# Optimization experiments

Hardware: AMD Instinct MI355X
Metric: run time of the kernel (lower is better)

## Reference

```python
import jax, jax.numpy as jnp
import numpy as np

D = 256; NH = 8; NL = 4; NP = 4; DH = D // NH; DFFN = 1024; NQ = 900; BS = 4
SPATIAL = ((92, 92), (46, 46), (23, 23), (12, 12))  # (H, W) per level
LEVEL_START = (0, 8464, 10580, 11109)
S = sum(h * w for h, w in SPATIAL)  # 11253


def _ln(x, g, b):
    m = jnp.mean(x, -1, keepdims=True)
    v = jnp.var(x, -1, keepdims=True)
    return (x - m) / jnp.sqrt(v + 1e-5) * g + b


def setup_inputs() -> dict:
    key = jax.random.key(0)
    ks = jax.random.split(key, 24)
    p = lambda k, s: 0.02 * jax.random.normal(k, s, jnp.float32)
    return {
        "tgt": jax.random.normal(ks[0], (NQ, BS, D), jnp.float32),
        "tgt_query_pos": jax.random.normal(ks[1], (NQ, BS, D), jnp.float32),
        "tgt_reference_points": jax.random.uniform(ks[2], (NQ, BS, NL, 2), jnp.float32),
        "memory": jax.random.normal(ks[3], (S, BS, D), jnp.float32),
        "memory_spatial_shapes": jnp.array(SPATIAL, jnp.int32),
        "memory_level_start_index": jnp.array(LEVEL_START, jnp.int32),
        "in_proj_w": p(ks[4], (3 * D, D)), "in_proj_b": p(ks[5], (3 * D,)),
        "out_proj_w": p(ks[6], (D, D)), "out_proj_b": p(ks[7], (D,)),
        "off_w": p(ks[8], (NH * NL * NP * 2, D)), "off_b": p(ks[9], (NH * NL * NP * 2,)),
        "aw_w": p(ks[10], (NH * NL * NP, D)), "aw_b": p(ks[11], (NH * NL * NP,)),
        "vproj_w": p(ks[12], (D, D)), "vproj_b": p(ks[13], (D,)),
        "oproj_w": p(ks[14], (D, D)), "oproj_b": p(ks[15], (D,)),
        "ln1_g": jnp.ones((D,), jnp.float32), "ln1_b": jnp.zeros((D,), jnp.float32),
        "ln2_g": jnp.ones((D,), jnp.float32), "ln2_b": jnp.zeros((D,), jnp.float32),
        "ln3_g": jnp.ones((D,), jnp.float32), "ln3_b": jnp.zeros((D,), jnp.float32),
        "lin1_w": p(ks[16], (DFFN, D)), "lin1_b": p(ks[17], (DFFN,)),
        "lin2_w": p(ks[18], (D, DFFN)), "lin2_b": p(ks[19], (D,)),
    }


def _self_attn(q, k, v, in_w, in_b, out_w, out_b):
    # q, k, v: (nq, bs, d) -- torch nn.MultiheadAttention, eval mode
    wq, wk, wv = jnp.split(in_w, 3, axis=0)
    bq, bk, bv = jnp.split(in_b, 3)
    qp = (q @ wq.T + bq).reshape(NQ, BS, NH, DH)
    kp = (k @ wk.T + bk).reshape(NQ, BS, NH, DH)
    vp = (v @ wv.T + bv).reshape(NQ, BS, NH, DH)
    s = jnp.einsum("qbhd,kbhd->bhqk", qp, kp) / jnp.sqrt(jnp.float32(DH))
    a = jax.nn.softmax(s, axis=-1)
    o = jnp.einsum("bhqk,kbhd->qbhd", a, vp).reshape(NQ, BS, D)
    return o @ out_w.T + out_b


def _msdeform(x, ref, mem, off_w, off_b, aw_w, aw_b, vproj_w, vproj_b, oproj_w, oproj_b):
    # x: (bs, nq, d); ref: (bs, nq, nl, 2) in [0,1]; mem: (bs, S, d)
    value = (mem @ vproj_w.T + vproj_b).reshape(BS, S, NH, DH)
    off = (x @ off_w.T + off_b).reshape(BS, NQ, NH, NL, NP, 2)
    aw = jax.nn.softmax((x @ aw_w.T + aw_b).reshape(BS, NQ, NH, NL * NP), axis=-1)
    aw = aw.reshape(BS, NQ, NH, NL, NP)
    # offset normalizer = (W, H) per level
    norm = jnp.array([[w, h] for (h, w) in SPATIAL], jnp.float32)
    loc = ref[:, :, None, :, None, :] + off / norm[None, None, None, :, None, :]
    out = jnp.zeros((BS, NH, NQ, DH), x.dtype)
    for l, (H, W) in enumerate(SPATIAL):
        s0 = LEVEL_START[l]
        v = value[:, s0:s0 + H * W].transpose(0, 2, 1, 3)  # (bs, nh, H*W, dh)
        g = loc[:, :, :, l].transpose(0, 2, 1, 3, 4)       # (bs, nh, nq, np, 2)
        # grid_sample align_corners=False, padding_mode='zeros'
        px = g[..., 0] * W - 0.5
        py = g[..., 1] * H - 0.5
        x0 = jnp.floor(px).astype(jnp.int32)
        y0 = jnp.floor(py).astype(jnp.int32)
        wx = px - x0
        wy = py - y0
        samp = jnp.zeros((BS, NH, NQ, NP, DH), x.dtype)
        for dx, dy, w in ((0, 0, (1 - wx) * (1 - wy)), (1, 0, wx * (1 - wy)),
                          (0, 1, (1 - wx) * wy), (1, 1, wx * wy)):
            xi = x0 + dx
            yi = y0 + dy
            valid = ((xi >= 0) & (xi < W) & (yi >= 0) & (yi < H)).astype(x.dtype)
            idx = (jnp.clip(yi, 0, H - 1) * W + jnp.clip(xi, 0, W - 1)).reshape(BS, NH, NQ * NP)
            gat = jnp.take_along_axis(v, idx[..., None], axis=2).reshape(BS, NH, NQ, NP, DH)
            samp = samp + (w * valid)[..., None] * gat
        a = aw[:, :, :, l].transpose(0, 2, 1, 3)  # (bs, nh, nq, np)
        out = out + (samp * a[..., None]).sum(axis=3)
    out = out.transpose(0, 2, 1, 3).reshape(BS, NQ, D)
    return out @ oproj_w.T + oproj_b


def reference(tgt, tgt_query_pos, tgt_reference_points, memory,
              memory_spatial_shapes, memory_level_start_index,
              in_proj_w, in_proj_b, out_proj_w, out_proj_b,
              off_w, off_b, aw_w, aw_b, vproj_w, vproj_b, oproj_w, oproj_b,
              ln1_g, ln1_b, ln2_g, ln2_b, ln3_g, ln3_b,
              lin1_w, lin1_b, lin2_w, lin2_b):
    # module_seq = ['sa', 'ca', 'ffn']; dropout inactive (eval)
    q = tgt + tgt_query_pos
    tgt2 = _self_attn(q, q, tgt, in_proj_w, in_proj_b, out_proj_w, out_proj_b)
    tgt = _ln(tgt + tgt2, ln2_g, ln2_b)
    x = (tgt + tgt_query_pos).transpose(1, 0, 2)
    ref = tgt_reference_points.transpose(1, 0, 2, 3)
    mem = memory.transpose(1, 0, 2)
    tgt2 = _msdeform(x, ref, mem, off_w, off_b, aw_w, aw_b,
                     vproj_w, vproj_b, oproj_w, oproj_b).transpose(1, 0, 2)
    tgt = _ln(tgt + tgt2, ln1_g, ln1_b)
    ff = jax.nn.relu(tgt @ lin1_w.T + lin1_b) @ lin2_w.T + lin2_b
    return _ln(tgt + ff, ln3_g, ln3_b)
```

## Files before the change

### kernel.cpp

```cpp
#include <hip/hip_runtime.h>
#include <math.h>

#define D_MODEL 256
#define NHEAD   8
#define NLVL    4
#define NPTS    4
#define DHEAD   32
#define DFFN    1024
#define NQ      900
#define BSZ     4
#define NROW    (NQ * BSZ)
#define NROWP   3648
#define S_TOT   11253
#define VROWS   (S_TOT * BSZ)
#define SASCALE 0.17677669529663687f

typedef __attribute__((ext_vector_type(8))) short short8;
typedef __attribute__((ext_vector_type(4))) float f32x4;
typedef unsigned short ushort_t;

static __device__ __forceinline__ unsigned f2bf1(float f) {
    unsigned u = __float_as_uint(f);
    return (u + 0x7FFFu + ((u >> 16) & 1u)) >> 16;
}
static __device__ __forceinline__ unsigned pack2bf(float x, float y) {
    return f2bf1(x) | (f2bf1(y) << 16);
}
static __device__ __forceinline__ float bf2f(ushort_t u) {
    return __uint_as_float(((unsigned)u) << 16);
}

#if __has_builtin(__builtin_amdgcn_global_load_lds)
#define HAS_GLL 1
#endif

static __device__ __forceinline__ void stage_w16(const ushort_t* g, ushort_t* ldsbase, int lane)
{
#ifdef HAS_GLL
    __builtin_amdgcn_global_load_lds(
        (const __attribute__((address_space(1))) unsigned int*)g,
        (__attribute__((address_space(3))) unsigned int*)ldsbase, 16, 0, 0);
#else
    *(uint4*)(ldsbase + lane * 8) = *(const uint4*)g;
#endif
}

#define WB_IN   0
#define WB_VP   196608
#define WB_OUTP 262144
#define WB_OFF  327680
#define WB_AW   393216
#define WB_OP   425984
#define WB_L1   491520
#define WB_L2   753664
#define WB_TOT  1015808

__global__ __launch_bounds__(256) void cvt_weights(
    const float* __restrict__ w_in, const float* __restrict__ w_vp,
    const float* __restrict__ w_outp, const float* __restrict__ w_off,
    const float* __restrict__ w_aw, const float* __restrict__ w_op,
    const float* __restrict__ w_l1, const float* __restrict__ w_l2,
    ushort_t* __restrict__ dst,
    const float* __restrict__ tgt, const float* __restrict__ qpos,
    ushort_t* __restrict__ tgt16, ushort_t* __restrict__ tq16)
{
    int b = blockIdx.x;
    if (b < 496) {
        const float* src;
        int dstoff;
        int kbits = 8;
        if (b < 96)       { src = w_in;   dstoff = WB_IN;   }
        else if (b < 128) { src = w_vp;   b -= 96;  dstoff = WB_VP;   }
        else if (b < 160) { src = w_outp; b -= 128; dstoff = WB_OUTP; }
        else if (b < 192) { src = w_off;  b -= 160; dstoff = WB_OFF;  }
        else if (b < 208) { src = w_aw;   b -= 192; dstoff = WB_AW;   }
        else if (b < 240) { src = w_op;   b -= 208; dstoff = WB_OP;   }
        else if (b < 368) { src = w_l1;   b -= 240; dstoff = WB_L1;   }
        else              { src = w_l2;   b -= 368; dstoff = WB_L2;   kbits = 10; }
        int i = (b * 256 + threadIdx.x) * 8;
        float4 f0 = *(const float4*)(src + i);
        float4 f1 = *(const float4*)(src + i + 4);
        uint4 u;
        u.x = pack2bf(f0.x, f0.y); u.y = pack2bf(f0.z, f0.w);
        u.z = pack2bf(f1.x, f1.y); u.w = pack2bf(f1.z, f1.w);
        int K = 1 << kbits;
        int n = i >> kbits;
        int k = i & (K - 1);
        int kswz = (k & ~63) | ((k & 63) ^ ((n & 7) << 3));
        *(uint4*)(dst + dstoff + (size_t)n * K + kswz) = u;
    } else {
        int bb = b - 496;
        ushort_t* dbuf = tgt16;
        bool addq = false;
        if (bb >= 456) { bb -= 456; dbuf = tq16; addq = true; }
        int i = bb * 2048 + threadIdx.x * 8;
        int row = i >> 8, k = i & 255;
        uint4 u = make_uint4(0u, 0u, 0u, 0u);
        if (row < NROW) {
            const float* sp = tgt + (size_t)row * 256 + k;
            float4 f0 = *(const float4*)(sp + 0);
            float4 f1 = *(const float4*)(sp + 4);
            if (addq) {
                const float* qp = qpos + (size_t)row * 256 + k;
                float4 q0 = *(const float4*)(qp + 0);
                float4 q1 = *(const float4*)(qp + 4);
                f0.x += q0.x; f0.y += q0.y; f0.z += q0.z; f0.w += q0.w;
                f1.x += q1.x; f1.y += q1.y; f1.z += q1.z; f1.w += q1.w;
            }
            u.x = pack2bf(f0.x, f0.y); u.y = pack2bf(f0.z, f0.w);
            u.z = pack2bf(f1.x, f1.y); u.w = pack2bf(f1.z, f1.w);
        }
        int kswz = (k & ~63) | ((k & 63) ^ ((row & 7) << 3));
        *(uint4*)(dbuf + (size_t)row * 256 + kswz) = u;
    }
}

__global__ __launch_bounds__(256) void proj_fused(
    const ushort_t* __restrict__ tq16, const ushort_t* __restrict__ tgt16,
    const ushort_t* __restrict__ in_wb, const float* __restrict__ in_b,
    const float* __restrict__ mem, const ushort_t* __restrict__ vp_wb,
    const float* __restrict__ vp_b,
    ushort_t* __restrict__ qkv16, ushort_t* __restrict__ value16)
{
    __shared__ ushort_t As[2][64 * 64];
    __shared__ ushort_t Ws[2][256 * 64];

    const int t    = threadIdx.x;
    const int bid  = blockIdx.x;
    const int wv   = t >> 6;
    const int ln   = t & 63;
    const int L    = ln & 15;
    const int quad = ln >> 4;
    const int swz  = (L & 7) << 3;
    const int lrow = ln >> 3;
    const int lchk = (ln & 7) << 3;

    if (bid < 684) {
        const int m0 = (bid % 57) * 64;
        const int n0 = (bid / 57) * 64;
        const float oscale = (n0 < 256) ? SASCALE : 1.f;
        const ushort_t* Ab = (n0 < 512) ? tq16 : tgt16;

        auto stageQ = [&](int k0, int buf) {
#pragma unroll
            for (int j = 0; j < 2; ++j) {
                int r0 = (wv * 2 + j) * 8;
                stage_w16(Ab + (size_t)(m0 + r0 + lrow) * 256 + k0 + lchk, &As[buf][r0 * 64], ln);
                stage_w16(in_wb + (size_t)(n0 + r0 + lrow) * 256 + k0 + lchk, &Ws[buf][r0 * 64], ln);
            }
        };

        f32x4 acc[4] = {{0.f,0.f,0.f,0.f},{0.f,0.f,0.f,0.f},
                        {0.f,0.f,0.f,0.f},{0.f,0.f,0.f,0.f}};

        stageQ(0, 0);
        __syncthreads();
        int cur = 0;
        for (int k = 0; k < 4; ++k) {
            if (k < 3) stageQ((k + 1) * 64, cur ^ 1);
#pragma unroll
            for (int kh = 0; kh < 2; ++kh) {
                int ko = (kh * 32 + quad * 8) ^ swz;
                short8 af = *(const short8*)&As[cur][(wv * 16 + L) * 64 + ko];
#pragma unroll
                for (int cb = 0; cb < 4; ++cb) {
                    short8 bf = *(const short8*)&Ws[cur][(cb * 16 + L) * 64 + ko];
                    acc[cb] = __builtin_amdgcn_mfma_f32_16x16x32_bf16(af, bf, acc[cb], 0, 0, 0);
                }
            }
            __syncthreads();
            cur ^= 1;
        }
#pragma unroll
        for (int cb = 0; cb < 4; ++cb) {
            int col = n0 + cb * 16 + L;
            float bv = in_b[col];
#pragma unroll
            for (int i = 0; i < 4; ++i) {
                int m = m0 + wv * 16 + quad * 4 + i;
                if (m < NROW)
                    qkv16[(size_t)m * 768 + col] = (ushort_t)f2bf1((acc[cb][i] + bv) * oscale);
            }
        }
    } else {
        const int vb = bid - 684;
        const int m0 = vb * 64;
        const int trow = t >> 2;
        const int tk   = (t & 3) << 4;
        const int wsz  = (trow & 7) << 3;

        const int  mrow = m0 + trow;
        const bool mv   = (mrow < VROWS);
        const float* arow = mem + (size_t)mrow * 256 + tk;

        auto stageWv = [&](int k0, int buf) {
#pragma unroll
            for (int j = 0; j < 8; ++j) {
                int r0 = (wv * 8 + j) * 8;
                stage_w16(vp_wb + (size_t)(r0 + lrow) * 256 + k0 + lchk, &Ws[buf][r0 * 64], ln);
            }
        };
        auto stageAv = [&](int k0, int buf) {
            uint4 u0, u1;
            if (mv) {
                const float* ap = arow + k0;
                float4 a0 = *(const float4*)(ap + 0);
                float4 a1 = *(const float4*)(ap + 4);
                float4 a2 = *(const float4*)(ap + 8);
                float4 a3 = *(const float4*)(ap + 12);
                u0.x = pack2bf(a0.x, a0.y); u0.y = pack2bf(a0.z, a0.w);
                u0.z = pack2bf(a1.x, a1.y); u0.w = pack2bf(a1.z, a1.w);
                u1.x = pack2bf(a2.x, a2.y); u1.y = pack2bf(a2.z, a2.w);
                u1.z = pack2bf(a3.x, a3.y); u1.w = pack2bf(a3.z, a3.w);
            } else {
                u0 = make_uint4(0u, 0u, 0u, 0u); u1 = u0;
            }
            *(uint4*)&As[buf][trow * 64 + (tk ^ wsz)]       = u0;
            *(uint4*)&As[buf][trow * 64 + ((tk + 8) ^ wsz)] = u1;
        };

        f32x4 acc[16];
#pragma unroll
        for (int i = 0; i < 16; ++i) acc[i] = (f32x4){0.f, 0.f, 0.f, 0.f};

        stageWv(0, 0);
        stageAv(0, 0);
        __syncthreads();
        int cur = 0;
        for (int k = 0; k < 4; ++k) {
            if (k < 3) stageWv((k + 1) * 64, cur ^ 1);
#pragma unroll
            for (int kh = 0; kh < 2; ++kh) {
                int ko = (kh * 32 + quad * 8) ^ swz;
                short8 af = *(const short8*)&As[cur][(wv * 16 + L) * 64 + ko];
#pragma unroll
                for (int cb = 0; cb < 16; ++cb) {
                    short8 bf = *(const short8*)&Ws[cur][(cb * 16 + L) * 64 + ko];
                    acc[cb] = __builtin_amdgcn_mfma_f32_16x16x32_bf16(af, bf, acc[cb], 0, 0, 0);
                }
            }
            if (k < 3) stageAv((k + 1) * 64, cur ^ 1);
            __syncthreads();
            cur ^= 1;
        }

        ushort_t* Cs = Ws[0];
#pragma unroll
        for (int half = 0; half < 2; ++half) {
            if (half) __syncthreads();
#pragma unroll
            for (int cb = 0; cb < 8; ++cb) {
                int col = cb * 16 + L;
                float bv = vp_b[half * 128 + col];
#pragma unroll
                for (int i = 0; i < 4; ++i) {
                    int r = wv * 16 + quad * 4 + i;
                    Cs[r * 136 + col] = (ushort_t)f2bf1(acc[half * 8 + cb][i] + bv);
                }
            }
            __syncthreads();
            {
                int r  = t >> 2;
                int ch = (t & 3) * 32;
                int m  = m0 + r;
                if (m < VROWS) {
                    const ushort_t* src = &Cs[r * 136 + ch];
                    uint4* dst = (uint4*)(value16 + (size_t)m * 256 + half * 128 + ch);
#pragma unroll
                    for (int j = 0; j < 4; ++j)
                        dst[j] = *(const uint4*)(src + j * 8);
                }
            }
        }
    }
}

__global__ __launch_bounds__(256) void sa_flash16(
    const ushort_t* __restrict__ qkv, ushort_t* __restrict__ attn_out)
{
    __shared__ ushort_t Ks[2 * 2080];
    __shared__ ushort_t Vt[2 * 2304];
    __shared__ ushort_t Ps[4 * 1152];

    const int t    = threadIdx.x;
    const int q0   = blockIdx.x * 64;
    const int b    = blockIdx.y & 3;
    const int h    = blockIdx.y >> 2;
    const int wv   = t >> 6;
    const int ln   = t & 63;
    const int L    = ln & 15;
    const int quad = ln >> 4;

    union { uint4 u; short8 s; } qu;
    qu.u = make_uint4(0u, 0u, 0u, 0u);
    {
        int q = q0 + wv * 16 + L;
        if (q < NQ)
            qu.u = *(const uint4*)(qkv + ((size_t)q * 4 + b) * 768 + h * 32 + quad * 8);
    }
    const short8 qf = qu.s;

    float mrun = -1e30f, lrun = 0.f;
    f32x4 oacc[2] = {{0.f,0.f,0.f,0.f},{0.f,0.f,0.f,0.f}};

    const int skey = t >> 2;
    const int sdg  = t & 3;

    uint4 ku, vu;
    auto kv_load = [&](int k0) {
        int kg = k0 + skey;
        ku = make_uint4(0u, 0u, 0u, 0u);
        vu = make_uint4(0u, 0u, 0u, 0u);
        if (kg < NQ) {
            const ushort_t* base = qkv + ((size_t)kg * 4 + b) * 768 + 256 + h * 32 + sdg * 8;
            ku = *(const uint4*)base;
            vu = *(const uint4*)(base + 256);
        }
    };

    kv_load(0);
    int it = 0;
    for (int k0 = 0; k0 < NQ; k0 += 64, it ^= 1) {
        *(uint4*)&Ks[it * 2080 + sdg * 520 + skey * 8] = ku;
        {
            ushort_t* vp = &Vt[it * 2304 + sdg * 8 * 72 + skey];
            vp[0 * 72] = (ushort_t)(vu.x & 0xffffu);
            vp[1 * 72] = (ushort_t)(vu.x >> 16);
            vp[2 * 72] = (ushort_t)(vu.y & 0xffffu);
            vp[3 * 72] = (ushort_t)(vu.y >> 16);
            vp[4 * 72] = (ushort_t)(vu.z & 0xffffu);
            vp[5 * 72] = (ushort_t)(vu.z >> 16);
            vp[6 * 72] = (ushort_t)(vu.w & 0xffffu);
            vp[7 * 72] = (ushort_t)(vu.w >> 16);
        }
        __syncthreads();
        if (k0 + 64 < NQ) kv_load(k0 + 64);

        f32x4 sacc[4] = {{0.f,0.f,0.f,0.f},{0.f,0.f,0.f,0.f},
                         {0.f,0.f,0.f,0.f},{0.f,0.f,0.f,0.f}};
#pragma unroll
        for (int cb = 0; cb < 4; ++cb) {
            short8 kf = *(const short8*)&Ks[it * 2080 + quad * 520 + (cb * 16 + L) * 8];
            sacc[cb] = __builtin_amdgcn_mfma_f32_16x16x32_bf16(kf, qf, sacc[cb], 0, 0, 0);
        }
        if (k0 + 64 > NQ) {
#pragma unroll
            for (int cb = 0; cb < 4; ++cb)
#pragma unroll
                for (int i = 0; i < 4; ++i)
                    if (k0 + cb * 16 + quad * 4 + i >= NQ) sacc[cb][i] = -1e30f;
        }

        float ml = -1e30f;
#pragma unroll
        for (int cb = 0; cb < 4; ++cb)
#pragma unroll
            for (int i = 0; i < 4; ++i) ml = fmaxf(ml, sacc[cb][i]);
        ml = fmaxf(ml, __shfl_xor(ml, 16, 64));
        ml = fmaxf(ml, __shfl_xor(ml, 32, 64));
        float mnew  = fmaxf(mrun, ml);
        float alpha = __expf(mrun - mnew);
        float p[16];
        float rs = 0.f;
#pragma unroll
        for (int cb = 0; cb < 4; ++cb)
#pragma unroll
            for (int i = 0; i < 4; ++i) {
                float e = __expf(sacc[cb][i] - mnew);
                p[cb * 4 + i] = e;
                rs += e;
            }
        rs += __shfl_xor(rs, 16, 64);
        rs += __shfl_xor(rs, 32, 64);
        lrun = lrun * alpha + rs;
        mrun = mnew;

        {
            ushort_t* pw = &Ps[wv * 1152 + L * 72];
#pragma unroll
            for (int cb = 0; cb < 4; ++cb) {
                uint2 u;
                u.x = pack2bf(p[cb * 4 + 0], p[cb * 4 + 1]);
                u.y = pack2bf(p[cb * 4 + 2], p[cb * 4 + 3]);
                *(uint2*)&pw[cb * 16 + quad * 4] = u;
            }
        }
#pragma unroll
        for (int i = 0; i < 4; ++i) {
            float ai = __shfl(alpha, quad * 4 + i, 64);
            oacc[0][i] *= ai;
            oacc[1][i] *= ai;
        }
        __syncthreads();

#pragma unroll
        for (int ks = 0; ks < 2; ++ks) {
            short8 pf = *(const short8*)&Ps[wv * 1152 + L * 72 + ks * 32 + quad * 8];
#pragma unroll
            for (int db = 0; db < 2; ++db) {
                short8 vf = *(const short8*)&Vt[it * 2304 + (db * 16 + L) * 72 + ks * 32 + quad * 8];
                oacc[db] = __builtin_amdgcn_mfma_f32_16x16x32_bf16(pf, vf, oacc[db], 0, 0, 0);
            }
        }
    }

#pragma unroll
    for (int i = 0; i < 4; ++i) {
        float lq = __shfl(lrun, quad * 4 + i, 64);
        float li = 1.f / lq;
        int q = q0 + wv * 16 + quad * 4 + i;
        if (q < NQ) {
            ushort_t* op = attn_out + ((size_t)q * 4 + b) * 256 + h * 32 + L;
            op[0]  = (ushort_t)f2bf1(oacc[0][i] * li);
            op[16] = (ushort_t)f2bf1(oacc[1][i] * li);
        }
    }
}

__global__ __launch_bounds__(512, 1) void fused_ca(
    const ushort_t* __restrict__ att16,
    const float* __restrict__ tgt, const float* __restrict__ qpos,
    const ushort_t* __restrict__ outp_wb, const float* __restrict__ outp_b,
    const float* __restrict__ ln2g, const float* __restrict__ ln2b,
    const ushort_t* __restrict__ off_wb, const float* __restrict__ off_b,
    const ushort_t* __restrict__ aw_wb, const float* __restrict__ aw_b,
    const float* __restrict__ refp,
    float* __restrict__ tgt_a, float* __restrict__ px_g,
    float* __restrict__ py_g, float* __restrict__ aw_g)
{
    __shared__ ushort_t Ws[2][256 * 64];
    __shared__ ushort_t att_s[16 * 264];
    __shared__ ushort_t xca_s[16 * 264];
    __shared__ float    aws_s[16 * 128];
    __shared__ float    sS[8][16], s2S[8][16];

    const int t    = threadIdx.x;
    const int m0   = blockIdx.x * 16;
    const int wv   = t >> 6;
    const int ln   = t & 63;
    const int L    = ln & 15;
    const int quad = ln >> 4;
    const int swz  = (L & 7) << 3;
    const int lrow = ln >> 3;
    const int lchk = (ln & 7) << 3;
    const int rloc = quad * 4;

    auto stage4 = [&](const ushort_t* base, int buf) {
#pragma unroll
        for (int j = 0; j < 4; ++j) {
            int r0 = (wv * 4 + j) * 8;
            stage_w16(base + (size_t)(r0 + lrow) * 256 + lchk, &Ws[buf][r0 * 64], ln);
        }
    };
    auto stage2 = [&](const ushort_t* base, int buf) {
#pragma unroll
        for (int j = 0; j < 2; ++j) {
            int r0 = (wv * 2 + j) * 8;
            stage_w16(base + (size_t)(r0 + lrow) * 256 + lchk, &Ws[buf][r0 * 64], ln);
        }
    };
    auto mfma2 = [&](const ushort_t* A, int koff, int buf, f32x4* acc) {
#pragma unroll
        for (int kh = 0; kh < 2; ++kh) {
            int ko = (kh * 32 + quad * 8) ^ swz;
            short8 af = *(const short8*)&A[L * 264 + koff + kh * 32 + quad * 8];
#pragma unroll
            for (int cb = 0; cb < 2; ++cb) {
                short8 bf = *(const short8*)&Ws[buf][(wv * 32 + cb * 16 + L) * 64 + ko];
                acc[cb] = __builtin_amdgcn_mfma_f32_16x16x32_bf16(af, bf, acc[cb], 0, 0, 0);
            }
        }
    };

    {
        int r = t >> 5, s = (t & 31) * 8;
        *(uint4*)&att_s[r * 264 + s] = *(const uint4*)(att16 + (size_t)(m0 + r) * 256 + s);
    }
    stage4(outp_wb, 0);
    __syncthreads();
    int cur = 0;

    {
        f32x4 acc[2] = {{0.f,0.f,0.f,0.f},{0.f,0.f,0.f,0.f}};
        for (int k = 0; k < 4; ++k) {
            if (k < 3) stage4(outp_wb + (k + 1) * 64, cur ^ 1);
            else       stage4(off_wb, cur ^ 1);
            mfma2(att_s, k * 64, cur, acc);
            __syncthreads();
            cur ^= 1;
        }
        float s[4] = {0.f,0.f,0.f,0.f}, s2v[4] = {0.f,0.f,0.f,0.f};
#pragma unroll
        for (int cb = 0; cb < 2; ++cb) {
            int col = wv * 32 + cb * 16 + L;
            float bv = outp_b[col];
#pragma unroll
            for (int i = 0; i < 4; ++i) {
                float xv = acc[cb][i] + bv + tgt[(size_t)(m0 + rloc + i) * 256 + col];
                acc[cb][i] = xv;
                s[i] += xv; s2v[i] += xv * xv;
            }
        }
#pragma unroll
        for (int off = 1; off < 16; off <<= 1)
#pragma unroll
            for (int i = 0; i < 4; ++i) {
                s[i]   += __shfl_xor(s[i],   off, 64);
                s2v[i] += __shfl_xor(s2v[i], off, 64);
            }
        if (L == 0)
#pragma unroll
            for (int i = 0; i < 4; ++i) { sS[wv][rloc + i] = s[i]; s2S[wv][rloc + i] = s2v[i]; }
        __syncthreads();
        float mean[4], rstd[4];
#pragma unroll
        for (int i = 0; i < 4; ++i) {
            float St = 0.f, S2t = 0.f;
#pragma unroll
            for (int w = 0; w < 8; ++w) { St += sS[w][rloc + i]; S2t += s2S[w][rloc + i]; }
            mean[i] = St * (1.f / 256.f);
            float var = S2t * (1.f / 256.f) - mean[i] * mean[i];
            rstd[i] = rsqrtf(var + 1e-5f);
        }
#pragma unroll
        for (int cb = 0; cb < 2; ++cb) {
            int col = wv * 32 + cb * 16 + L;
            float gv = ln2g[col], bt = ln2b[col];
#pragma unroll
            for (int i = 0; i < 4; ++i) {
                float y = (acc[cb][i] - mean[i]) * rstd[i] * gv + bt;
                tgt_a[(size_t)(m0 + rloc + i) * 256 + col] = y;
                xca_s[(rloc + i) * 264 + col] =
                    (ushort_t)f2bf1(y + qpos[(size_t)(m0 + rloc + i) * 256 + col]);
            }
        }
        __syncthreads();
    }

    {
        f32x4 acc[2] = {{0.f,0.f,0.f,0.f},{0.f,0.f,0.f,0.f}};
        for (int k = 0; k < 4; ++k) {
            if (k < 3) stage4(off_wb + (k + 1) * 64, cur ^ 1);
            else       stage2(aw_wb, cur ^ 1);
            mfma2(xca_s, k * 64, cur, acc);
            __syncthreads();
            cur ^= 1;
        }
        const float dims[4] = {92.f, 46.f, 23.f, 12.f};
#pragma unroll
        for (int cb = 0; cb < 2; ++cb) {
            int col = wv * 32 + cb * 16 + L;
            float bv = off_b[col];
            int hh = col >> 5, lp = (col & 31) >> 1, isY = col & 1;
            int l = lp >> 2;
            float dim = dims[l];
            float* dst = isY ? py_g : px_g;
#pragma unroll
            for (int i = 0; i < 4; ++i) {
                int row = m0 + rloc + i;
                float ref = refp[((size_t)row * 4 + l) * 2 + isY];
                dst[(size_t)row * 128 + hh * 16 + lp] = ref * dim + (acc[cb][i] + bv) - 0.5f;
            }
        }
    }

    {
        f32x4 acc = {0.f, 0.f, 0.f, 0.f};
        for (int k = 0; k < 4; ++k) {
            if (k < 3) stage2(aw_wb + (k + 1) * 64, cur ^ 1);
#pragma unroll
            for (int kh = 0; kh < 2; ++kh) {
                int ko = (kh * 32 + quad * 8) ^ swz;
                short8 af = *(const short8*)&xca_s[L * 264 + k * 64 + kh * 32 + quad * 8];
                short8 bf = *(const short8*)&Ws[cur][(wv * 16 + L) * 64 + ko];
                acc = __builtin_amdgcn_mfma_f32_16x16x32_bf16(af, bf, acc, 0, 0, 0);
            }
            __syncthreads();
            cur ^= 1;
        }
        {
            int col = wv * 16 + L;
            float bv = aw_b[col];
#pragma unroll
            for (int i = 0; i < 4; ++i)
                aws_s[(rloc + i) * 128 + col] = acc[i] + bv;
        }
        __syncthreads();
    }

    if (t < 128) {
        int r = t >> 3, hh = t & 7;
        float v[16];
        float m = -1e30f;
#pragma unroll
        for (int j = 0; j < 16; ++j) { v[j] = aws_s[r * 128 + hh * 16 + j]; m = fmaxf(m, v[j]); }
        float ssum = 0.f;
#pragma unroll
        for (int j = 0; j < 16; ++j) { v[j] = __expf(v[j] - m); ssum += v[j]; }
        float inv = 1.f / ssum;
#pragma unroll
        for (int j = 0; j < 16; ++j)
            aw_g[(size_t)(m0 + r) * 128 + hh * 16 + j] = v[j] * inv;
    }
}

__global__ __launch_bounds__(256) void msdeform4(
    const float* __restrict__ px_g, const float* __restrict__ py_g,
    const float* __restrict__ aw_g, const ushort_t* __restrict__ value16,
    ushort_t* __restrict__ out)
{
    const int t   = threadIdx.x;
    const int row = blockIdx.x * 4 + (t >> 6);
    const int ln  = t & 63;
    const int h   = ln >> 3;
    const int d   = (ln & 7) * 4;
    const int b   = row & 3;

    const int HsI[4] = {92, 46, 23, 12};
    const int S0_[4] = {0, 8464, 10580, 11109};

    const ushort_t* vb = value16 + (size_t)b * 256 + h * 32 + d;
    const float* pxr = px_g + (size_t)row * 128 + h * 16;
    const float* pyr = py_g + (size_t)row * 128 + h * 16;
    const float* awr = aw_g + (size_t)row * 128 + h * 16;

    float a0 = 0.f, a1 = 0.f, a2 = 0.f, a3 = 0.f;
#pragma unroll
    for (int l = 0; l < 4; ++l) {
        const int H = HsI[l], W = HsI[l], base = S0_[l];
#pragma unroll
        for (int p = 0; p < 4; ++p) {
            const int lp = l * 4 + p;
            float px = pxr[lp], py = pyr[lp], aw = awr[lp];
            float x0f = floorf(px), y0f = floorf(py);
            int x0 = (int)x0f, y0 = (int)y0f;
            float wx = px - x0f, wy = py - y0f;
            float s0 = 0.f, s1 = 0.f, s2 = 0.f, s3 = 0.f;
#pragma unroll
            for (int dy = 0; dy < 2; ++dy) {
#pragma unroll
                for (int dx = 0; dx < 2; ++dx) {
                    int xi = x0 + dx, yi = y0 + dy;
                    float flag = (xi >= 0 && xi < W && yi >= 0 && yi < H) ? 1.f : 0.f;
                    int xc = xi < 0 ? 0 : (xi >= W ? W - 1 : xi);
                    int yc = yi < 0 ? 0 : (yi >= H ? H - 1 : yi);
                    float wgt = (dx ? wx : 1.f - wx) * (dy ? wy : 1.f - wy) * flag;
                    uint2 gv = *(const uint2*)(vb + (size_t)(base + yc * W + xc) * 1024);
                    s0 = fmaf(wgt, bf2f((ushort_t)(gv.x & 0xffffu)), s0);
                    s1 = fmaf(wgt, bf2f((ushort_t)(gv.x >> 16)), s1);
                    s2 = fmaf(wgt, bf2f((ushort_t)(gv.y & 0xffffu)), s2);
                    s3 = fmaf(wgt, bf2f((ushort_t)(gv.y >> 16)), s3);
                }
            }
            a0 = fmaf(aw, s0, a0);
            a1 = fmaf(aw, s1, a1);
            a2 = fmaf(aw, s2, a2);
            a3 = fmaf(aw, s3, a3);
        }
    }
    uint2 u;
    u.x = pack2bf(a0, a1);
    u.y = pack2bf(a2, a3);
    *(uint2*)(out + (size_t)row * 256 + h * 32 + d) = u;
}

__global__ __launch_bounds__(512, 1) void ffn_fused(
    const ushort_t* __restrict__ att2_16,
    const float* __restrict__ tgt_a,
    const ushort_t* __restrict__ op_wb, const float* __restrict__ op_b,
    const float* __restrict__ ln1g, const float* __restrict__ ln1b,
    const ushort_t* __restrict__ l1_wb, const float* __restrict__ l1b,
    const ushort_t* __restrict__ l2_wb, const float* __restrict__ l2b,
    const float* __restrict__ ln3g, const float* __restrict__ ln3b,
    float* __restrict__ out)
{
    __shared__ ushort_t Ws[2][256 * 64];
    __shared__ ushort_t A1[16 * 264];
    __shared__ ushort_t hc[16 * 264];
    __shared__ float    sS[8][16], s2S[8][16];

    const int t    = threadIdx.x;
    const int m0   = blockIdx.x * 16;
    const int wv   = t >> 6;
    const int ln   = t & 63;
    const int L    = ln & 15;
    const int quad = ln >> 4;
    const int swz  = (L & 7) << 3;
    const int lrow = ln >> 3;
    const int lchk = (ln & 7) << 3;
    const int rloc = quad * 4;

    auto stageWs = [&](const ushort_t* base, int stride, int buf) {
#pragma unroll
        for (int j = 0; j < 4; ++j) {
            int r0 = (wv * 4 + j) * 8;
            stage_w16(base + (size_t)(r0 + lrow) * stride + lchk, &Ws[buf][r0 * 64], ln);
        }
    };
    auto mfma2 = [&](const ushort_t* A, int koff, int buf, f32x4* acc) {
#pragma unroll
        for (int kh = 0; kh < 2; ++kh) {
            int ko = (kh * 32 + quad * 8) ^ swz;
            short8 af = *(const short8*)&A[L * 264 + koff + kh * 32 + quad * 8];
#pragma unroll
            for (int cb = 0; cb < 2; ++cb) {
                short8 bf = *(const short8*)&Ws[buf][(wv * 32 + cb * 16 + L) * 64 + ko];
                acc[cb] = __builtin_amdgcn_mfma_f32_16x16x32_bf16(af, bf, acc[cb], 0, 0, 0);
            }
        }
    };

    {
        int r = t >> 5, s = (t & 31) * 8;
        *(uint4*)&hc[r * 264 + s] = *(const uint4*)(att2_16 + (size_t)(m0 + r) * 256 + s);
    }
    stageWs(op_wb, 256, 0);
    __syncthreads();
    int cur = 0;

    f32x4 resid[2];

    {
        f32x4 acc[2] = {{0.f,0.f,0.f,0.f},{0.f,0.f,0.f,0.f}};
        for (int k = 0; k < 4; ++k) {
            if (k < 3) stageWs(op_wb + (k + 1) * 64, 256, cur ^ 1);
            else       stageWs(l1_wb, 256, cur ^ 1);
            mfma2(hc, k * 64, cur, acc);
            __syncthreads();
            cur ^= 1;
        }
        float s[4] = {0.f,0.f,0.f,0.f}, s2v[4] = {0.f,0.f,0.f,0.f};
#pragma unroll
        for (int cb = 0; cb < 2; ++cb) {
            int col = wv * 32 + cb * 16 + L;
            float bv = op_b[col];
#pragma unroll
            for (int i = 0; i < 4; ++i) {
                float xv = acc[cb][i] + bv + tgt_a[(size_t)(m0 + rloc + i) * 256 + col];
                acc[cb][i] = xv;
                s[i] += xv; s2v[i] += xv * xv;
            }
        }
#pragma unroll
        for (int off = 1; off < 16; off <<= 1)
#pragma unroll
            for (int i = 0; i < 4; ++i) {
                s[i]   += __shfl_xor(s[i],   off, 64);
                s2v[i] += __shfl_xor(s2v[i], off, 64);
            }
        if (L == 0)
#pragma unroll
            for (int i = 0; i < 4; ++i) { sS[wv][rloc + i] = s[i]; s2S[wv][rloc + i] = s2v[i]; }
        __syncthreads();
        float mean[4], rstd[4];
#pragma unroll
        for (int i = 0; i < 4; ++i) {
            float St = 0.f, S2t = 0.f;
#pragma unroll
            for (int w = 0; w < 8; ++w) { St += sS[w][rloc + i]; S2t += s2S[w][rloc + i]; }
            mean[i] = St * (1.f / 256.f);
            float var = S2t * (1.f / 256.f) - mean[i] * mean[i];
            rstd[i] = rsqrtf(var + 1e-5f);
        }
#pragma unroll
        for (int cb = 0; cb < 2; ++cb) {
            int col = wv * 32 + cb * 16 + L;
            float gv = ln1g[col], bt = ln1b[col];
#pragma unroll
            for (int i = 0; i < 4; ++i) {
                float y = (acc[cb][i] - mean[i]) * rstd[i] * gv + bt;
                resid[cb][i] = y;
                A1[(rloc + i) * 264 + col] = (ushort_t)f2bf1(y);
            }
        }
        __syncthreads();
    }

    f32x4 accf[2] = {{0.f,0.f,0.f,0.f},{0.f,0.f,0.f,0.f}};
    for (int c = 0; c < 4; ++c) {
        f32x4 acch[2] = {{0.f,0.f,0.f,0.f},{0.f,0.f,0.f,0.f}};
        for (int k = 0; k < 4; ++k) {
            if (k < 3) stageWs(l1_wb + (size_t)(c * 256) * 256 + (k + 1) * 64, 256, cur ^ 1);
            else       stageWs(l2_wb + c * 256, 1024, cur ^ 1);
            mfma2(A1, k * 64, cur, acch);
            __syncthreads();
            cur ^= 1;
        }
#pragma unroll
        for (int cb = 0; cb < 2; ++cb) {
            int colc = wv * 32 + cb * 16 + L;
            float bv = l1b[c * 256 + colc];
#pragma unroll
            for (int i = 0; i < 4; ++i)
                hc[(rloc + i) * 264 + colc] = (ushort_t)f2bf1(fmaxf(acch[cb][i] + bv, 0.f));
        }
        __syncthreads();
        for (int k = 0; k < 4; ++k) {
            if (k < 3)      stageWs(l2_wb + c * 256 + (k + 1) * 64, 1024, cur ^ 1);
            else if (c < 3) stageWs(l1_wb + (size_t)((c + 1) * 256) * 256, 256, cur ^ 1);
            mfma2(hc, k * 64, cur, accf);
            __syncthreads();
            cur ^= 1;
        }
    }

    {
        float s[4] = {0.f,0.f,0.f,0.f}, s2v[4] = {0.f,0.f,0.f,0.f};
#pragma unroll
        for (int cb = 0; cb < 2; ++cb) {
            int col = wv * 32 + cb * 16 + L;
            float bv = l2b[col];
#pragma unroll
            for (int i = 0; i < 4; ++i) {
                float xv = accf[cb][i] + bv + resid[cb][i];
                accf[cb][i] = xv;
                s[i] += xv; s2v[i] += xv * xv;
            }
        }
#pragma unroll
        for (int off = 1; off < 16; off <<= 1)
#pragma unroll
            for (int i = 0; i < 4; ++i) {
                s[i]   += __shfl_xor(s[i],   off, 64);
                s2v[i] += __shfl_xor(s2v[i], off, 64);
            }
        if (L == 0)
#pragma unroll
            for (int i = 0; i < 4; ++i) { sS[wv][rloc + i] = s[i]; s2S[wv][rloc + i] = s2v[i]; }
        __syncthreads();
        float mean[4], rstd[4];
#pragma unroll
        for (int i = 0; i < 4; ++i) {
            float St = 0.f, S2t = 0.f;
#pragma unroll
            for (int w = 0; w < 8; ++w) { St += sS[w][rloc + i]; S2t += s2S[w][rloc + i]; }
            mean[i] = St * (1.f / 256.f);
            float var = S2t * (1.f / 256.f) - mean[i] * mean[i];
            rstd[i] = rsqrtf(var + 1e-5f);
        }
#pragma unroll
        for (int cb = 0; cb < 2; ++cb) {
            int col = wv * 32 + cb * 16 + L;
            float gv = ln3g[col], bt = ln3b[col];
#pragma unroll
            for (int i = 0; i < 4; ++i) {
                float y = (accf[cb][i] - mean[i]) * rstd[i] * gv + bt;
                out[(size_t)(m0 + rloc + i) * 256 + col] = y;
            }
        }
    }
}

extern "C" void kernel_launch(void* const* d_in, const int* in_sizes, int n_in,
                              void* d_out, int out_size, void* d_ws, size_t ws_size,
                              hipStream_t stream)
{
    const float* tgt    = (const float*)d_in[0];
    const float* qpos   = (const float*)d_in[1];
    const float* refp   = (const float*)d_in[2];
    const float* mem    = (const float*)d_in[3];
    const float* in_w   = (const float*)d_in[6];
    const float* in_b   = (const float*)d_in[7];
    const float* outp_w = (const float*)d_in[8];
    const float* outp_b = (const float*)d_in[9];
    const float* off_w  = (const float*)d_in[10];
    const float* off_b  = (const float*)d_in[11];
    const float* aw_w   = (const float*)d_in[12];
    const float* aw_b   = (const float*)d_in[13];
    const float* vp_w   = (const float*)d_in[14];
    const float* vp_b   = (const float*)d_in[15];
    const float* op_w   = (const float*)d_in[16];
    const float* op_b   = (const float*)d_in[17];
    const float* ln1g   = (const float*)d_in[18];
    const float* ln1b   = (const float*)d_in[19];
    const float* ln2g   = (const float*)d_in[20];
    const float* ln2b   = (const float*)d_in[21];
    const float* ln3g   = (const float*)d_in[22];
    const float* ln3b   = (const float*)d_in[23];
    const float* l1w    = (const float*)d_in[24];
    const float* l1b    = (const float*)d_in[25];
    const float* l2w    = (const float*)d_in[26];
    const float* l2b    = (const float*)d_in[27];
    float* out = (float*)d_out;
    float* ws  = (float*)d_ws;

    ushort_t* qkv16    = (ushort_t*)ws;
    ushort_t* att16    = (ushort_t*)(ws + 691200);
    float*    tgt_a    = ws + 1843200;
    ushort_t* tgt16    = (ushort_t*)(ws + 1843200);
    ushort_t* tq16     = (ushort_t*)(ws + 2310144);
    float*    px_g     = ws + 2995200;
    float*    py_g     = ws + 3456000;
    float*    aw_g     = ws + 3916800;
    ushort_t* att2_16  = (ushort_t*)(ws + 4377600);
    ushort_t* value16  = (ushort_t*)(ws + 5760000);
    ushort_t* wb       = (ushort_t*)(ws + 13364736);

    const ushort_t* in_wb   = wb + WB_IN;
    const ushort_t* vp_wb   = wb + WB_VP;
    const ushort_t* outp_wb = wb + WB_OUTP;
    const ushort_t* off_wb  = wb + WB_OFF;
    const ushort_t* aw_wb   = wb + WB_AW;
    const ushort_t* op_wb   = wb + WB_OP;
    const ushort_t* l1_wb   = wb + WB_L1;
    const ushort_t* l2_wb   = wb + WB_L2;

    dim3 b256(256);

    hipLaunchKernelGGL(cvt_weights, dim3(1408), b256, 0, stream,
                       in_w, vp_w, outp_w, off_w, aw_w, op_w, l1w, l2w, wb,
                       tgt, qpos, tgt16, tq16);
    hipLaunchKernelGGL(proj_fused, dim3(1388), b256, 0, stream,
                       tq16, tgt16, in_wb, in_b, mem, vp_wb, vp_b, qkv16, value16);
    hipLaunchKernelGGL(sa_flash16, dim3(15, 32), b256, 0, stream, qkv16, att16);
    hipLaunchKernelGGL(fused_ca, dim3(225), dim3(512), 0, stream,
                       att16, tgt, qpos, outp_wb, outp_b, ln2g, ln2b,
                       off_wb, off_b, aw_wb, aw_b, refp,
                       tgt_a, px_g, py_g, aw_g);
    hipLaunchKernelGGL(msdeform4, dim3(900), b256, 0, stream,
                       px_g, py_g, aw_g, value16, att2_16);
    hipLaunchKernelGGL(ffn_fused, dim3(225), dim3(512), 0, stream,
                       att2_16, tgt_a, op_wb, op_b, ln1g, ln1b,
                       l1_wb, l1b, l2_wb, l2b, ln3g, ln3b, out);
}
```

Measured before the change: 248.6 us.

## Replace syncthreads with explicit vmcnt waits and raw barriers in GEMM pipelines

Replaces __syncthreads in the double-buffered GEMM loops with hand-placed s_waitcnt vmcnt(N) plus s_barrier. The wait lets the prefetch for the next K-slice stay in flight while the current slice is consumed, so loads and compute can overlap. Several barriers that look redundant are removed or reduced to lgkmcnt-only waits. This relies on exact counts of outstanding global loads per thread. If a count is wrong, or if stageAv's register-path loads are mixed in, it risks races on the shared buffers.

```diff
diff --git a/kernel.cpp b/kernel.cpp
--- a/kernel.cpp
+++ b/kernel.cpp
@@ -44,6 +44,16 @@
     *(uint4*)(ldsbase + lane * 8) = *(const uint4*)g;
 #endif
 }
+
+#define WAIT_VM_BAR(N) do {                                            \
+    asm volatile("s_waitcnt vmcnt(" #N ") lgkmcnt(0)" ::: "memory");   \
+    __builtin_amdgcn_sched_barrier(0);                                 \
+    __builtin_amdgcn_s_barrier(); } while (0)
+
+#define LK_BAR() do {                                                  \
+    asm volatile("s_waitcnt lgkmcnt(0)" ::: "memory");                 \
+    __builtin_amdgcn_sched_barrier(0);                                 \
+    __builtin_amdgcn_s_barrier(); } while (0)
 
 #define WB_IN   0
 #define WB_VP   196608
@@ -154,10 +164,10 @@
                         {0.f,0.f,0.f,0.f},{0.f,0.f,0.f,0.f}};
 
         stageQ(0, 0);
-        __syncthreads();
         int cur = 0;
         for (int k = 0; k < 4; ++k) {
-            if (k < 3) stageQ((k + 1) * 64, cur ^ 1);
+            if (k < 3) { stageQ((k + 1) * 64, cur ^ 1); WAIT_VM_BAR(4); }
+            else       { WAIT_VM_BAR(0); }
 #pragma unroll
             for (int kh = 0; kh < 2; ++kh) {
                 int ko = (kh * 32 + quad * 8) ^ swz;
@@ -168,7 +178,7 @@
                     acc[cb] = __builtin_amdgcn_mfma_f32_16x16x32_bf16(af, bf, acc[cb], 0, 0, 0);
                 }
             }
-            __syncthreads();
+            __builtin_amdgcn_s_barrier();
             cur ^= 1;
         }
 #pragma unroll
@@ -225,10 +235,10 @@
 
         stageWv(0, 0);
         stageAv(0, 0);
-        __syncthreads();
         int cur = 0;
         for (int k = 0; k < 4; ++k) {
-            if (k < 3) stageWv((k + 1) * 64, cur ^ 1);
+            if (k < 3) { stageWv((k + 1) * 64, cur ^ 1); WAIT_VM_BAR(8); }
+            else       { WAIT_VM_BAR(0); }
 #pragma unroll
             for (int kh = 0; kh < 2; ++kh) {
                 int ko = (kh * 32 + quad * 8) ^ swz;
@@ -240,7 +250,7 @@
                 }
             }
             if (k < 3) stageAv((k + 1) * 64, cur ^ 1);
-            __syncthreads();
+            __builtin_amdgcn_s_barrier();
             cur ^= 1;
         }
 
@@ -477,7 +487,6 @@
         *(uint4*)&att_s[r * 264 + s] = *(const uint4*)(att16 + (size_t)(m0 + r) * 256 + s);
     }
     stage4(outp_wb, 0);
-    __syncthreads();
     int cur = 0;
 
     {
@@ -485,8 +494,9 @@
         for (int k = 0; k < 4; ++k) {
             if (k < 3) stage4(outp_wb + (k + 1) * 64, cur ^ 1);
             else       stage4(off_wb, cur ^ 1);
+            WAIT_VM_BAR(4);
             mfma2(att_s, k * 64, cur, acc);
-            __syncthreads();
+            __builtin_amdgcn_s_barrier();
             cur ^= 1;
         }
         float s[4] = {0.f,0.f,0.f,0.f}, s2v[4] = {0.f,0.f,0.f,0.f};
@@ -511,7 +521,7 @@
         if (L == 0)
 #pragma unroll
             for (int i = 0; i < 4; ++i) { sS[wv][rloc + i] = s[i]; s2S[wv][rloc + i] = s2v[i]; }
-        __syncthreads();
+        LK_BAR();
         float mean[4], rstd[4];
 #pragma unroll
         for (int i = 0; i < 4; ++i) {
@@ -534,16 +544,15 @@
                     (ushort_t)f2bf1(y + qpos[(size_t)(m0 + rloc + i) * 256 + col]);
             }
         }
-        __syncthreads();
     }
 
     {
         f32x4 acc[2] = {{0.f,0.f,0.f,0.f},{0.f,0.f,0.f,0.f}};
         for (int k = 0; k < 4; ++k) {
-            if (k < 3) stage4(off_wb + (k + 1) * 64, cur ^ 1);
-            else       stage2(aw_wb, cur ^ 1);
+            if (k < 3) { stage4(off_wb + (k + 1) * 64, cur ^ 1); WAIT_VM_BAR(4); }
+            else       { stage2(aw_wb, cur ^ 1);                 WAIT_VM_BAR(2); }
             mfma2(xca_s, k * 64, cur, acc);
-            __syncthreads();
+            __builtin_amdgcn_s_barrier();
             cur ^= 1;
         }
         const float dims[4] = {92.f, 46.f, 23.f, 12.f};
@@ -567,7 +576,8 @@
     {
         f32x4 acc = {0.f, 0.f, 0.f, 0.f};
         for (int k = 0; k < 4; ++k) {
-            if (k < 3) stage2(aw_wb + (k + 1) * 64, cur ^ 1);
+            if (k < 3) { stage2(aw_wb + (k + 1) * 64, cur ^ 1); WAIT_VM_BAR(2); }
+            else       { WAIT_VM_BAR(0); }
 #pragma unroll
             for (int kh = 0; kh < 2; ++kh) {
                 int ko = (kh * 32 + quad * 8) ^ swz;
@@ -575,7 +585,7 @@
                 short8 bf = *(const short8*)&Ws[cur][(wv * 16 + L) * 64 + ko];
                 acc = __builtin_amdgcn_mfma_f32_16x16x32_bf16(af, bf, acc, 0, 0, 0);
             }
-            __syncthreads();
+            __builtin_amdgcn_s_barrier();
             cur ^= 1;
         }
         {
@@ -585,7 +595,7 @@
             for (int i = 0; i < 4; ++i)
                 aws_s[(rloc + i) * 128 + col] = acc[i] + bv;
         }
-        __syncthreads();
+        LK_BAR();
     }
 
     if (t < 128) {
@@ -715,7 +725,6 @@
         *(uint4*)&hc[r * 264 + s] = *(const uint4*)(att2_16 + (size_t)(m0 + r) * 256 + s);
     }
     stageWs(op_wb, 256, 0);
-    __syncthreads();
     int cur = 0;
 
     f32x4 resid[2];
@@ -725,8 +734,9 @@
         for (int k = 0; k < 4; ++k) {
             if (k < 3) stageWs(op_wb + (k + 1) * 64, 256, cur ^ 1);
             else       stageWs(l1_wb, 256, cur ^ 1);
+            WAIT_VM_BAR(4);
             mfma2(hc, k * 64, cur, acc);
-            __syncthreads();
+            __builtin_amdgcn_s_barrier();
             cur ^= 1;
         }
         float s[4] = {0.f,0.f,0.f,0.f}, s2v[4] = {0.f,0.f,0.f,0.f};
@@ -751,7 +761,7 @@
         if (L == 0)
 #pragma unroll
             for (int i = 0; i < 4; ++i) { sS[wv][rloc + i] = s[i]; s2S[wv][rloc + i] = s2v[i]; }
-        __syncthreads();
+        LK_BAR();
         float mean[4], rstd[4];
 #pragma unroll
         for (int i = 0; i < 4; ++i) {
@@ -773,7 +783,6 @@
                 A1[(rloc + i) * 264 + col] = (ushort_t)f2bf1(y);
             }
         }
-        __syncthreads();
     }
 
     f32x4 accf[2] = {{0.f,0.f,0.f,0.f},{0.f,0.f,0.f,0.f}};
@@ -782,8 +791,9 @@
         for (int k = 0; k < 4; ++k) {
             if (k < 3) stageWs(l1_wb + (size_t)(c * 256) * 256 + (k + 1) * 64, 256, cur ^ 1);
             else       stageWs(l2_wb + c * 256, 1024, cur ^ 1);
+            WAIT_VM_BAR(4);
             mfma2(A1, k * 64, cur, acch);
-            __syncthreads();
+            __builtin_amdgcn_s_barrier();
             cur ^= 1;
         }
 #pragma unroll
@@ -794,12 +804,13 @@
             for (int i = 0; i < 4; ++i)
                 hc[(rloc + i) * 264 + colc] = (ushort_t)f2bf1(fmaxf(acch[cb][i] + bv, 0.f));
         }
-        __syncthreads();
+        LK_BAR();
         for (int k = 0; k < 4; ++k) {
-            if (k < 3)      stageWs(l2_wb + c * 256 + (k + 1) * 64, 1024, cur ^ 1);
-            else if (c < 3) stageWs(l1_wb + (size_t)((c + 1) * 256) * 256, 256, cur ^ 1);
+            if (k < 3)      { stageWs(l2_wb + c * 256 + (k + 1) * 64, 1024, cur ^ 1); WAIT_VM_BAR(4); }
+            else if (c < 3) { stageWs(l1_wb + (size_t)((c + 1) * 256) * 256, 256, cur ^ 1); WAIT_VM_BAR(4); }
+            else            { WAIT_VM_BAR(0); }
             mfma2(hc, k * 64, cur, accf);
-            __syncthreads();
+            __builtin_amdgcn_s_barrier();
             cur ^= 1;
         }
     }
@@ -827,7 +838,7 @@
         if (L == 0)
 #pragma unroll
             for (int i = 0; i < 4; ++i) { sS[wv][rloc + i] = s[i]; s2S[wv][rloc + i] = s2v[i]; }
-        __syncthreads();
+        LK_BAR();
         float mean[4], rstd[4];
 #pragma unroll
         for (int i = 0; i < 4; ++i) {
```

Result: faster. 242.9 us (-2.3%).
